# Performance work log

Measured on AMD Instinct MI355X. Metric: run time of the kernel, lower is better.

## Reference

```python
import jax, jax.numpy as jnp
import numpy as np
from jax import lax

# ---- static module constants (the torch module's registered buffers) ----
NRB = 8            # num_radial_basis
RAD = 2.5          # diameter / 2
GRID = 192         # voxel grid extent
N = 200000         # occupied voxels
DIM = 80           # 32x0e + 16x1o
ALPHA = 1.0 / np.sqrt(48.0)   # e3nn path normalization (fan_in = 32 + 16 into each output irrep)

_ax = np.arange(-2.0, 3.0, dtype=np.float32)                        # floor(2.5/1.0)=2 -> 5 taps/axis
LATTICE = np.stack(np.meshgrid(_ax, _ax, _ax, indexing='ij'), -1)   # [5,5,5,3]
PERM = np.arange(125).reshape(5, 5, 5).transpose(2, 1, 0).reshape(-1)  # einsum('xyz...->zyx...') as a flat permutation
OFFS = LATTICE.reshape(-1, 3).astype(np.int32)[PERM]                # voxel offsets, ordered to match permuted kernel


def _radial_emb():
    # soft_one_hot_linspace(..., basis='smooth_finite', cutoff=True)
    d = np.linalg.norm(LATTICE, axis=-1)
    centers = np.linspace(0.0, RAD, NRB + 2)[1:-1]
    step = centers[1] - centers[0]
    t = (d[..., None] - centers) / step
    inside = np.abs(t) < 1.0
    safe = np.where(inside, 1.0 - t * t, 1.0)
    return (1.14136 * np.exp(2.0) * np.where(inside, np.exp(-2.0 / safe), 0.0)).astype(np.float32)

EMB = _radial_emb().reshape(-1, NRB)  # [125, 8]


def _sph():
    # spherical harmonics l=0,1; normalize=True, normalization='component' (|Y_l|^2 = 2l+1)
    n = np.linalg.norm(LATTICE, axis=-1, keepdims=True)
    u = np.where(n > 0, LATTICE / np.maximum(n, 1e-9), 0.0)
    return np.concatenate([np.ones_like(n), np.sqrt(3.0) * u], -1).astype(np.float32)

SH = _sph().reshape(-1, 4)  # [125, 4]


def make_kernel(weight):
    # kernel(): (emb @ weight) / numel(lattice), then tp.right(sh, w) -> [tap, dim_in, dim_out]
    w = jnp.asarray(EMB) @ weight / 125.0        # [125, 2304]
    w1 = w[:, :1024].reshape(125, 32, 32)        # path 0e x 0e -> 0e
    w2 = w[:, 1024:1536].reshape(125, 32, 16)    # path 0e x 1o -> 1o
    w3 = w[:, 1536:1792].reshape(125, 16, 16)    # path 1o x 0e -> 1o
    w4 = w[:, 1792:].reshape(125, 16, 32)        # path 1o x 1o -> 0e (dot product)
    s0 = jnp.asarray(SH[:, 0])
    v = jnp.asarray(SH[:, 1:])
    eye3 = jnp.eye(3, dtype=w.dtype)
    K00 = ALPHA * w1 * s0[:, None, None]                                                  # [125,32,32]
    K01 = ALPHA * jnp.einsum('pik,pm->pikm', w2, v).reshape(125, 32, 48)                  # [125,32,48]
    K11 = ALPHA * jnp.einsum('pik,mn->pimkn', w3 * s0[:, None, None], eye3).reshape(125, 48, 48)
    K10 = (ALPHA / np.sqrt(3.0)) * jnp.einsum('pik,pm->pimk', w4, v).reshape(125, 48, 32)
    K = jnp.concatenate([jnp.concatenate([K00, K01], 2), jnp.concatenate([K10, K11], 2)], 1)
    return K[jnp.asarray(PERM)]  # xyz -> zyx tap order + flatten


def _forward(feats, weight, w_sc0, w_sc1, coords):
    kern = make_kernel(weight)  # [125, 80, 80]
    # residual e3nn Linear: per-irrep channel mixing with 1/sqrt(fan_in) normalization
    sc0 = feats[:, :32] @ (w_sc0 / np.sqrt(32.0))
    sc1 = jnp.einsum('nim,ik->nkm', feats[:, 32:].reshape(-1, 16, 3), w_sc1 / np.sqrt(16.0)).reshape(-1, 48)
    sc = jnp.concatenate([sc0, sc1], -1)
    # Minkowski sparse voxel conv: dense index volume -> per-tap gather / GEMM / accumulate
    n = coords.shape[0]
    idx_vol = jnp.full((GRID, GRID, GRID), -1, jnp.int32)
    idx_vol = idx_vol.at[coords[:, 0], coords[:, 1], coords[:, 2]].set(jnp.arange(n, dtype=jnp.int32))

    def tap(acc, oK):
        off, Ko = oK
        c = coords + off                                  # [N,3] neighbor coords for this tap
        ok = jnp.all((c >= 0) & (c < GRID), axis=1)
        cc = jnp.clip(c, 0, GRID - 1)
        nb = idx_vol[cc[:, 0], cc[:, 1], cc[:, 2]]        # [N] row index or -1
        f = jnp.where((ok & (nb >= 0))[:, None], feats[jnp.maximum(nb, 0)], 0.0)
        return acc + f @ Ko, None

    out, _ = lax.scan(tap, jnp.zeros(feats.shape, feats.dtype), (jnp.asarray(OFFS), kern))
    return sc + out


def setup_inputs() -> dict:
    key = jax.random.key(0)
    k1, k2, k3, k4 = jax.random.split(key, 4)
    rng = np.random.default_rng(0)
    lin = rng.choice(GRID ** 3, size=N, replace=False)  # unique occupied voxels
    coords = np.stack([lin // (GRID * GRID), (lin // GRID) % GRID, lin % GRID], 1).astype(np.int32)
    return {
        'feats': jax.random.normal(k1, (N, DIM), jnp.float32),
        'weight': jax.random.normal(k2, (NRB, 2304), jnp.float32),
        'w_sc0': jax.random.normal(k3, (32, 32), jnp.float32),
        'w_sc1': jax.random.normal(k4, (16, 16), jnp.float32),
        'coords': jnp.asarray(coords),
    }


def reference(feats, weight, w_sc0, w_sc1, coords):
    return _forward(feats, weight, w_sc0, w_sc1, coords)
```

## Files before the change

### kernel.cpp

```cpp
#include <hip/hip_runtime.h>

#define N_PTS 200000
#define GRIDL 192
#define CAP 8192
#define NREG 216
#define RCAP 1152
#define SCAP 96
#define HMAX 16
#define HCAP_TOT 524288

#define VOL_OFF   0ull
#define VOL_BYTES (192ull*192ull*192ull*4ull)
#define BINS_OFF  28311552ull
#define BCNT_OFF  36503552ull
#define GCUR_OFF  36519552ull
#define RCNT_OFF  36519680ull
#define PLIST_OFF 36547328ull
#define WBUF_OFF  38537984ull
#define VTAB_OFF  39689984ull
#define A0_OFF    39691984ull
#define A1_OFF    39696080ull
#define HDR_OFF   39697104ull
#define STAGE_OFF 41297104ull
#define WS_NEED   (STAGE_OFF + (unsigned long long)HCAP_TOT * 320ull)

struct TapTable { int p[80]; };
__host__ __device__ constexpr TapTable make_taps() {
    TapTable tt{}; int t = 0;
    for (int a = -2; a <= 2; a++)
        for (int b = -2; b <= 2; b++)
            for (int c = -2; c <= 2; c++) {
                int sq = a*a + b*b + c*c;
                if (sq >= 1 && sq <= 6) tt.p[t++] = (a+2)*25 + (b+2)*5 + (c+2);
            }
    return tt;
}
__device__ const TapTable TAPS = make_taps();

__global__ void prep_kernel(const float* __restrict__ wt, const float* __restrict__ wsc0,
                            const float* __restrict__ wsc1, float* __restrict__ wbuf,
                            float* __restrict__ vtab, float* __restrict__ A0,
                            float* __restrict__ A1) {
    int p = blockIdx.x;
    int dx = p / 25 - 2, dy = (p / 5) % 5 - 2, dz = p % 5 - 2;
    double d = sqrt((double)(dx*dx + dy*dy + dz*dz));
    const double step = 2.5 / 9.0;
    const double cst = 1.14136 * exp(2.0);
    float emb[8];
#pragma unroll
    for (int r = 0; r < 8; r++) {
        double t = (d - (double)(r + 1) * step) / step;
        double tt = t * t;
        emb[r] = (tt < 1.0) ? (float)(cst * exp(-2.0 / (1.0 - tt))) : 0.0f;
    }
    if (threadIdx.x == 0) {
        float inv = (d > 0.0) ? (float)(sqrt(3.0) / d) : 0.0f;
        vtab[p*4+0] = dx * inv; vtab[p*4+1] = dy * inv;
        vtab[p*4+2] = dz * inv; vtab[p*4+3] = 0.0f;
    }
    const float ALPHA = 0.14433756729740643f;
    for (int q = threadIdx.x; q < 2304; q += blockDim.x) {
        float acc = 0.0f;
#pragma unroll
        for (int r = 0; r < 8; r++) acc = fmaf(emb[r], wt[r*2304 + q], acc);
        acc *= (1.0f / 125.0f);
        float val = acc * ((q < 1792) ? ALPHA : (1.0f / 12.0f));
        wbuf[p*2304 + q] = val;
        if (p == 62) {
            if (q < 1024)                   A0[q]        = wsc0[q] * 0.17677669529663687f + val;
            else if (q >= 1536 && q < 1792) A1[q-1536]   = wsc1[q-1536] * 0.25f + val;
        }
    }
}

__global__ __launch_bounds__(256) void scatter_kernel(const int* __restrict__ coords,
        int* __restrict__ vol, int* __restrict__ rcnt_pad, int2* __restrict__ plist) {
    __shared__ int hist[216];
    __shared__ int rbase[216];
    for (int i = threadIdx.x; i < 216; i += 256) hist[i] = 0;
    __syncthreads();
    for (int n = blockIdx.x * 256 + threadIdx.x; n < N_PTS; n += 65536) {
        int x = coords[n*3], y = coords[n*3+1], z = coords[n*3+2];
        vol[(x * GRIDL + y) * GRIDL + z] = n;
        int r = (x >> 5) * 36 + (y >> 5) * 6 + (z >> 5);
        atomicAdd(&hist[r], 1);
    }
    __syncthreads();
    if (threadIdx.x < 216) {
        rbase[threadIdx.x] = atomicAdd(&rcnt_pad[threadIdx.x * 32], hist[threadIdx.x]);
        hist[threadIdx.x] = 0;
    }
    __syncthreads();
    for (int n = blockIdx.x * 256 + threadIdx.x; n < N_PTS; n += 65536) {
        int x = coords[n*3], y = coords[n*3+1], z = coords[n*3+2];
        int r = (x >> 5) * 36 + (y >> 5) * 6 + (z >> 5);
        int j = rbase[r] + atomicAdd(&hist[r], 1);
        if (j < RCAP) plist[r * RCAP + j] = make_int2(n, (x << 16) | (y << 8) | z);
    }
}

template<bool STG>
__global__ __launch_bounds__(256) void enum_kernel(const int* __restrict__ vol,
        const int* __restrict__ rcnt_pad, const int2* __restrict__ plist,
        int* __restrict__ bcnt_pad, int2* __restrict__ bins,
        int2* __restrict__ hdr, int* __restrict__ gcur) {
    int r = blockIdx.x;
    int cnt = min(rcnt_pad[r * 32], RCAP);
    __shared__ int hist[80];
    __shared__ int tbase[80];
    __shared__ int2 stage[80][SCAP];
    __shared__ int2 mh[STG ? 256 * HMAX : 1];
    __shared__ int blockTot;
    __shared__ int gbase_s;
    for (int i = threadIdx.x; i < 80; i += 256) hist[i] = 0;
    __syncthreads();

    for (int base = 0; base < cnt; base += 256) {
        int idx = base + threadIdx.x;
        bool act = idx < cnt;
        int n = -1, x = 0, y = 0, z = 0;
        if (act) {
            int2 e = plist[r * RCAP + idx];
            n = e.x; x = e.y >> 16; y = (e.y >> 8) & 255; z = e.y & 255;
        }
        int myc = 0;
        int t = 0;
#pragma unroll
        for (int a = -2; a <= 2; a++)
#pragma unroll
        for (int b = -2; b <= 2; b++)
#pragma unroll
        for (int c = -2; c <= 2; c++) {
            int sq = a*a + b*b + c*c;
            if (sq < 1 || sq > 6) continue;
            int cx = x + a, cy = y + b, cz = z + c;
            if (act && ((unsigned)cx < 192u) && ((unsigned)cy < 192u) && ((unsigned)cz < 192u)) {
                int nb = vol[(cx * GRIDL + cy) * GRIDL + cz];
                if (nb >= 0) {
                    if (STG) {
                        if (myc < HMAX) mh[threadIdx.x * HMAX + myc] = make_int2(t, nb);
                        myc++;
                    } else {
                        int j = atomicAdd(&hist[t], 1);
                        if (j < SCAP) stage[t][j] = make_int2(n, nb);
                    }
                }
            }
            t++;
        }
        if (STG) {
            myc = min(myc, HMAX);
            __syncthreads();
            if (threadIdx.x == 0) blockTot = 0;
            __syncthreads();
            int lbase = atomicAdd(&blockTot, myc);
            __syncthreads();
            if (threadIdx.x == 0) gbase_s = atomicAdd(gcur, blockTot);
            __syncthreads();
            int sbase = gbase_s + lbase;
            int avail = HCAP_TOT - sbase;
            int cn = min(myc, max(avail, 0));
            if (act) hdr[n] = make_int2(sbase, cn);
            for (int j = 0; j < cn; j++) {
                int2 e = mh[threadIdx.x * HMAX + j];
                int k = atomicAdd(&hist[e.x], 1);
                if (k < SCAP) stage[e.x][k] = make_int2(sbase + j, e.y);
            }
            __syncthreads();
        }
    }
    __syncthreads();
    if (threadIdx.x < 80) {
        int c = min(hist[threadIdx.x], SCAP);
        tbase[threadIdx.x] = atomicAdd(&bcnt_pad[TAPS.p[threadIdx.x] * 32], c);
    }
    __syncthreads();
    for (int t2 = 0; t2 < 80; t2++) {
        int c = min(hist[t2], SCAP);
        if (threadIdx.x < c) {
            int slot = tbase[t2] + threadIdx.x;
            if (slot < CAP) bins[TAPS.p[t2] * CAP + slot] = stage[t2][threadIdx.x];
        }
    }
}

__global__ __launch_bounds__(256) void sc_self_kernel(const float* __restrict__ feats,
        const float* __restrict__ A0, const float* __restrict__ A1,
        float* __restrict__ out) {
    __shared__ __align__(16) float sA0[1024];
    __shared__ __align__(16) float sA1[256];
    for (int i = threadIdx.x; i < 1024; i += 256) sA0[i] = A0[i];
    if (threadIdx.x < 256) sA1[threadIdx.x] = A1[threadIdx.x];
    __syncthreads();
    int n = blockIdx.x * 256 + threadIdx.x;
    if (n >= N_PTS) return;
    const float4* fr = (const float4*)(feats + (size_t)n * 80);
    float4* orow = (float4*)(out + (size_t)n * 80);
    float f0[32];
#pragma unroll
    for (int j = 0; j < 8; j++) {
        float4 t = fr[j];
        f0[4*j] = t.x; f0[4*j+1] = t.y; f0[4*j+2] = t.z; f0[4*j+3] = t.w;
    }
    float a0[32];
#pragma unroll
    for (int k = 0; k < 32; k++) a0[k] = 0.0f;
#pragma unroll
    for (int i = 0; i < 32; i++) {
        float fv = f0[i];
#pragma unroll
        for (int k4 = 0; k4 < 8; k4++) {
            float4 w = ((const float4*)sA0)[i*8 + k4];
            a0[4*k4]   = fmaf(fv, w.x, a0[4*k4]);
            a0[4*k4+1] = fmaf(fv, w.y, a0[4*k4+1]);
            a0[4*k4+2] = fmaf(fv, w.z, a0[4*k4+2]);
            a0[4*k4+3] = fmaf(fv, w.w, a0[4*k4+3]);
        }
    }
#pragma unroll
    for (int j = 0; j < 8; j++) orow[j] = make_float4(a0[4*j], a0[4*j+1], a0[4*j+2], a0[4*j+3]);
    float f1[48];
#pragma unroll
    for (int j = 0; j < 12; j++) {
        float4 t = fr[8 + j];
        f1[4*j] = t.x; f1[4*j+1] = t.y; f1[4*j+2] = t.z; f1[4*j+3] = t.w;
    }
    float a1[48];
#pragma unroll
    for (int k = 0; k < 48; k++) a1[k] = 0.0f;
#pragma unroll
    for (int i = 0; i < 16; i++) {
        float fm0 = f1[3*i], fm1 = f1[3*i+1], fm2 = f1[3*i+2];
#pragma unroll
        for (int k4 = 0; k4 < 4; k4++) {
            float4 w = ((const float4*)sA1)[i*4 + k4];
            const float* wp = (const float*)&w;
#pragma unroll
            for (int kk = 0; kk < 4; kk++) {
                int k = 4*k4 + kk;
                a1[3*k]   = fmaf(fm0, wp[kk], a1[3*k]);
                a1[3*k+1] = fmaf(fm1, wp[kk], a1[3*k+1]);
                a1[3*k+2] = fmaf(fm2, wp[kk], a1[3*k+2]);
            }
        }
    }
#pragma unroll
    for (int j = 0; j < 12; j++) orow[8+j] = make_float4(a1[4*j], a1[4*j+1], a1[4*j+2], a1[4*j+3]);
}

template<bool STG>
__global__ __launch_bounds__(128) void bin_kernel(const float* __restrict__ feats,
        const float* __restrict__ wbuf, const float* __restrict__ vtab,
        const int* __restrict__ bcnt_pad, const int2* __restrict__ bins,
        float* __restrict__ stg, float* __restrict__ out) {
    int p = blockIdx.x >> 4;
    int chunk = blockIdx.x & 15;
    int cnt = min(bcnt_pad[p * 32], CAP);
    int start = chunk * 512;
    if (start >= cnt) return;

    __shared__ __align__(16) float sW[2304];
    __shared__ float sv[4];
    __shared__ float ystage[2][64][81];
    __shared__ int   dst[2][64];

    for (int i = threadIdx.x; i < 2304; i += 128) sW[i] = wbuf[p*2304 + i];
    if (threadIdx.x < 4) sv[threadIdx.x] = vtab[p*4 + threadIdx.x];
    __syncthreads();

    int wv = threadIdx.x >> 6, lane = threadIdx.x & 63;
    const float4* sW1 = (const float4*)sW;
    const float4* sW2 = (const float4*)(sW + 1024);
    const float4* sW3 = (const float4*)(sW + 1536);
    const float4* sW4 = (const float4*)(sW + 1792);
    float v0 = sv[0], v1 = sv[1], v2 = sv[2];

    for (int it = 0; it < 4; it++) {
        int h = start + it * 128 + threadIdx.x;
        bool act = h < cnt;
        int d = -1, nb = 0;
        if (act) { int2 e = bins[p*CAP + h]; d = e.x; nb = e.y; }

        const float4* fr = (const float4*)(feats + (size_t)nb * 80);
        float f0[32], f1[48];
#pragma unroll
        for (int j = 0; j < 8; j++) {
            float4 t = fr[j];
            f0[4*j] = t.x; f0[4*j+1] = t.y; f0[4*j+2] = t.z; f0[4*j+3] = t.w;
        }
#pragma unroll
        for (int j = 0; j < 12; j++) {
            float4 t = fr[8 + j];
            f1[4*j] = t.x; f1[4*j+1] = t.y; f1[4*j+2] = t.z; f1[4*j+3] = t.w;
        }
        float g[16];
#pragma unroll
        for (int i = 0; i < 16; i++)
            g[i] = f1[3*i]*v0 + f1[3*i+1]*v1 + f1[3*i+2]*v2;

        float a0[32], cc[16];
#pragma unroll
        for (int k = 0; k < 32; k++) a0[k] = 0.0f;
#pragma unroll
        for (int k = 0; k < 16; k++) cc[k] = 0.0f;
#pragma unroll
        for (int i = 0; i < 32; i++) {
            float fv = f0[i];
#pragma unroll
            for (int k4 = 0; k4 < 8; k4++) {
                float4 w = sW1[i*8 + k4];
                a0[4*k4]   = fmaf(fv, w.x, a0[4*k4]);
                a0[4*k4+1] = fmaf(fv, w.y, a0[4*k4+1]);
                a0[4*k4+2] = fmaf(fv, w.z, a0[4*k4+2]);
                a0[4*k4+3] = fmaf(fv, w.w, a0[4*k4+3]);
            }
#pragma unroll
            for (int k4 = 0; k4 < 4; k4++) {
                float4 w = sW2[i*4 + k4];
                cc[4*k4]   = fmaf(fv, w.x, cc[4*k4]);
                cc[4*k4+1] = fmaf(fv, w.y, cc[4*k4+1]);
                cc[4*k4+2] = fmaf(fv, w.z, cc[4*k4+2]);
                cc[4*k4+3] = fmaf(fv, w.w, cc[4*k4+3]);
            }
        }
#pragma unroll
        for (int i = 0; i < 16; i++) {
            float gv = g[i];
#pragma unroll
            for (int k4 = 0; k4 < 8; k4++) {
                float4 w = sW4[i*8 + k4];
                a0[4*k4]   = fmaf(gv, w.x, a0[4*k4]);
                a0[4*k4+1] = fmaf(gv, w.y, a0[4*k4+1]);
                a0[4*k4+2] = fmaf(gv, w.z, a0[4*k4+2]);
                a0[4*k4+3] = fmaf(gv, w.w, a0[4*k4+3]);
            }
        }
#pragma unroll
        for (int k = 0; k < 32; k++) ystage[wv][lane][k] = a0[k];

        float a1[48];
#pragma unroll
        for (int k = 0; k < 16; k++) {
            a1[3*k] = v0 * cc[k]; a1[3*k+1] = v1 * cc[k]; a1[3*k+2] = v2 * cc[k];
        }
#pragma unroll
        for (int i = 0; i < 16; i++) {
            float fm0 = f1[3*i], fm1 = f1[3*i+1], fm2 = f1[3*i+2];
#pragma unroll
            for (int k4 = 0; k4 < 4; k4++) {
                float4 w = sW3[i*4 + k4];
                const float* wp = (const float*)&w;
#pragma unroll
                for (int kk = 0; kk < 4; kk++) {
                    int k = 4*k4 + kk;
                    a1[3*k]   = fmaf(fm0, wp[kk], a1[3*k]);
                    a1[3*k+1] = fmaf(fm1, wp[kk], a1[3*k+1]);
                    a1[3*k+2] = fmaf(fm2, wp[kk], a1[3*k+2]);
                }
            }
        }
#pragma unroll
        for (int k = 0; k < 48; k++) ystage[wv][lane][32 + k] = a1[k];
        dst[wv][lane] = act ? d : -1;
        __syncthreads();

        for (int h2 = 0; h2 < 64; h2++) {
            int dd = dst[wv][h2];
            if (dd < 0) continue;
            if (STG) {
                float* row = stg + (size_t)dd * 80;
                row[lane] = ystage[wv][h2][lane];
                if (lane < 16) row[64 + lane] = ystage[wv][h2][64 + lane];
            } else {
                float* orow = out + (size_t)dd * 80;
                unsafeAtomicAdd(orow + lane, ystage[wv][h2][lane]);
                if (lane < 16) unsafeAtomicAdd(orow + 64 + lane, ystage[wv][h2][64 + lane]);
            }
        }
        __syncthreads();
    }
}

__global__ __launch_bounds__(256) void gather_kernel(const float* __restrict__ feats,
        const float* __restrict__ A0, const float* __restrict__ A1,
        const int2* __restrict__ hdr, const float* __restrict__ stg,
        float* __restrict__ out) {
    __shared__ __align__(16) float sA0[1024];
    __shared__ __align__(16) float sA1[256];
    for (int i = threadIdx.x; i < 1024; i += 256) sA0[i] = A0[i];
    if (threadIdx.x < 256) sA1[threadIdx.x] = A1[threadIdx.x];
    __syncthreads();
    int n = blockIdx.x * 256 + threadIdx.x;
    if (n >= N_PTS) return;
    int2 h = hdr[n];
    const float4* fr = (const float4*)(feats + (size_t)n * 80);
    float a0[32], a1[48];
    {
        float f0[32];
#pragma unroll
        for (int j = 0; j < 8; j++) {
            float4 t = fr[j];
            f0[4*j] = t.x; f0[4*j+1] = t.y; f0[4*j+2] = t.z; f0[4*j+3] = t.w;
        }
#pragma unroll
        for (int k = 0; k < 32; k++) a0[k] = 0.0f;
#pragma unroll
        for (int i = 0; i < 32; i++) {
            float fv = f0[i];
#pragma unroll
            for (int k4 = 0; k4 < 8; k4++) {
                float4 w = ((const float4*)sA0)[i*8 + k4];
                a0[4*k4]   = fmaf(fv, w.x, a0[4*k4]);
                a0[4*k4+1] = fmaf(fv, w.y, a0[4*k4+1]);
                a0[4*k4+2] = fmaf(fv, w.z, a0[4*k4+2]);
                a0[4*k4+3] = fmaf(fv, w.w, a0[4*k4+3]);
            }
        }
        float f1[48];
#pragma unroll
        for (int j = 0; j < 12; j++) {
            float4 t = fr[8 + j];
            f1[4*j] = t.x; f1[4*j+1] = t.y; f1[4*j+2] = t.z; f1[4*j+3] = t.w;
        }
#pragma unroll
        for (int k = 0; k < 48; k++) a1[k] = 0.0f;
#pragma unroll
        for (int i = 0; i < 16; i++) {
            float fm0 = f1[3*i], fm1 = f1[3*i+1], fm2 = f1[3*i+2];
#pragma unroll
            for (int k4 = 0; k4 < 4; k4++) {
                float4 w = ((const float4*)sA1)[i*4 + k4];
                const float* wp = (const float*)&w;
#pragma unroll
                for (int kk = 0; kk < 4; kk++) {
                    int k = 4*k4 + kk;
                    a1[3*k]   = fmaf(fm0, wp[kk], a1[3*k]);
                    a1[3*k+1] = fmaf(fm1, wp[kk], a1[3*k+1]);
                    a1[3*k+2] = fmaf(fm2, wp[kk], a1[3*k+2]);
                }
            }
        }
    }
    for (int j = 0; j < h.y; j++) {
        const float4* rp = (const float4*)(stg + (size_t)(h.x + j) * 80);
#pragma unroll
        for (int q = 0; q < 8; q++) {
            float4 t = rp[q];
            a0[4*q] += t.x; a0[4*q+1] += t.y; a0[4*q+2] += t.z; a0[4*q+3] += t.w;
        }
#pragma unroll
        for (int q = 0; q < 12; q++) {
            float4 t = rp[8 + q];
            a1[4*q] += t.x; a1[4*q+1] += t.y; a1[4*q+2] += t.z; a1[4*q+3] += t.w;
        }
    }
    float4* orow = (float4*)(out + (size_t)n * 80);
#pragma unroll
    for (int j = 0; j < 8; j++)  orow[j]   = make_float4(a0[4*j], a0[4*j+1], a0[4*j+2], a0[4*j+3]);
#pragma unroll
    for (int j = 0; j < 12; j++) orow[8+j] = make_float4(a1[4*j], a1[4*j+1], a1[4*j+2], a1[4*j+3]);
}

extern "C" void kernel_launch(void* const* d_in, const int* in_sizes, int n_in,
                              void* d_out, int out_size, void* d_ws, size_t ws_size,
                              hipStream_t stream) {
    const float* feats = (const float*)d_in[0];
    const float* wt    = (const float*)d_in[1];
    const float* wsc0  = (const float*)d_in[2];
    const float* wsc1  = (const float*)d_in[3];
    const int*   coords= (const int*)d_in[4];
    float* out = (float*)d_out;
    char* ws = (char*)d_ws;

    int*   vol      = (int*)(ws + VOL_OFF);
    int2*  bins     = (int2*)(ws + BINS_OFF);
    int*   bcnt_pad = (int*)(ws + BCNT_OFF);
    int*   gcur     = (int*)(ws + GCUR_OFF);
    int*   rcnt_pad = (int*)(ws + RCNT_OFF);
    int2*  plist    = (int2*)(ws + PLIST_OFF);
    float* wbuf     = (float*)(ws + WBUF_OFF);
    float* vtab     = (float*)(ws + VTAB_OFF);
    float* A0       = (float*)(ws + A0_OFF);
    float* A1       = (float*)(ws + A1_OFF);
    int2*  hdr      = (int2*)(ws + HDR_OFF);
    float* stg      = (float*)(ws + STAGE_OFF);

    bool staging = (unsigned long long)ws_size >= WS_NEED;

    hipMemsetAsync(vol, 0xFF, VOL_BYTES, stream);
    hipMemsetAsync(bcnt_pad, 0, 16000 + 128 + 27648, stream);

    prep_kernel<<<125, 256, 0, stream>>>(wt, wsc0, wsc1, wbuf, vtab, A0, A1);
    scatter_kernel<<<256, 256, 0, stream>>>(coords, vol, rcnt_pad, plist);
    if (staging) {
        enum_kernel<true><<<NREG, 256, 0, stream>>>(vol, rcnt_pad, plist, bcnt_pad, bins, hdr, gcur);
        bin_kernel<true><<<125 * 16, 128, 0, stream>>>(feats, wbuf, vtab, bcnt_pad, bins, stg, out);
        gather_kernel<<<(N_PTS + 255) / 256, 256, 0, stream>>>(feats, A0, A1, hdr, stg, out);
    } else {
        enum_kernel<false><<<NREG, 256, 0, stream>>>(vol, rcnt_pad, plist, bcnt_pad, bins, hdr, gcur);
        sc_self_kernel<<<(N_PTS + 255) / 256, 256, 0, stream>>>(feats, A0, A1, out);
        bin_kernel<false><<<125 * 16, 128, 0, stream>>>(feats, wbuf, vtab, bcnt_pad, bins, stg, out);
    }
}
```

Baseline: 514.9 us.

## Split neighbor enumeration across region slices and write bin outputs directly

Neighbor enumeration now runs one 128-thread block per 128-point slice of each region instead of one 256-thread block per region. This spreads 216 large blocks over many more small ones, and the per-tap shared staging array gives way to a packed per-thread list with a two-pass count-then-place scheme. The bin kernel drops the shared-memory transpose and barrier-heavy per-row writeback: each thread writes its staged row with float4 stores, or with per-element atomics on the fallback path. Costs are more global atomics on the bin counters, less coalesced row stores, and packing that assumes neighbor indices fit in 18 bits.

Result: slower. 718.8 us (+39.6%).

```diff
diff --git a/kernel.cpp b/kernel.cpp
--- a/kernel.cpp
+++ b/kernel.cpp
@@ -5,7 +5,7 @@
 #define CAP 8192
 #define NREG 216
 #define RCAP 1152
-#define SCAP 96
+#define NSLICE 9
 #define HMAX 16
 #define HCAP_TOT 524288
 
@@ -87,7 +87,8 @@
     }
     __syncthreads();
     if (threadIdx.x < 216) {
-        rbase[threadIdx.x] = atomicAdd(&rcnt_pad[threadIdx.x * 32], hist[threadIdx.x]);
+        int c = hist[threadIdx.x];
+        rbase[threadIdx.x] = c ? atomicAdd(&rcnt_pad[threadIdx.x * 32], c) : 0;
         hist[threadIdx.x] = 0;
     }
     __syncthreads();
@@ -100,87 +101,77 @@
 }
 
 template<bool STG>
-__global__ __launch_bounds__(256) void enum_kernel(const int* __restrict__ vol,
+__global__ __launch_bounds__(128) void enum_kernel(const int* __restrict__ vol,
         const int* __restrict__ rcnt_pad, const int2* __restrict__ plist,
         int* __restrict__ bcnt_pad, int2* __restrict__ bins,
         int2* __restrict__ hdr, int* __restrict__ gcur) {
-    int r = blockIdx.x;
+    int r = blockIdx.x / NSLICE, s = blockIdx.x % NSLICE;
     int cnt = min(rcnt_pad[r * 32], RCAP);
+    int lo = s * 128, hi = min(cnt, lo + 128);
+    if (lo >= hi) return;
     __shared__ int hist[80];
     __shared__ int tbase[80];
-    __shared__ int2 stage[80][SCAP];
-    __shared__ int2 mh[STG ? 256 * HMAX : 1];
-    __shared__ int blockTot;
-    __shared__ int gbase_s;
-    for (int i = threadIdx.x; i < 80; i += 256) hist[i] = 0;
-    __syncthreads();
-
-    for (int base = 0; base < cnt; base += 256) {
-        int idx = base + threadIdx.x;
-        bool act = idx < cnt;
-        int n = -1, x = 0, y = 0, z = 0;
-        if (act) {
-            int2 e = plist[r * RCAP + idx];
-            n = e.x; x = e.y >> 16; y = (e.y >> 8) & 255; z = e.y & 255;
-        }
-        int myc = 0;
-        int t = 0;
-#pragma unroll
-        for (int a = -2; a <= 2; a++)
-#pragma unroll
-        for (int b = -2; b <= 2; b++)
-#pragma unroll
-        for (int c = -2; c <= 2; c++) {
-            int sq = a*a + b*b + c*c;
-            if (sq < 1 || sq > 6) continue;
-            int cx = x + a, cy = y + b, cz = z + c;
-            if (act && ((unsigned)cx < 192u) && ((unsigned)cy < 192u) && ((unsigned)cz < 192u)) {
-                int nb = vol[(cx * GRIDL + cy) * GRIDL + cz];
-                if (nb >= 0) {
-                    if (STG) {
-                        if (myc < HMAX) mh[threadIdx.x * HMAX + myc] = make_int2(t, nb);
-                        myc++;
-                    } else {
-                        int j = atomicAdd(&hist[t], 1);
-                        if (j < SCAP) stage[t][j] = make_int2(n, nb);
-                    }
-                }
-            }
-            t++;
-        }
-        if (STG) {
-            myc = min(myc, HMAX);
-            __syncthreads();
-            if (threadIdx.x == 0) blockTot = 0;
-            __syncthreads();
-            int lbase = atomicAdd(&blockTot, myc);
-            __syncthreads();
-            if (threadIdx.x == 0) gbase_s = atomicAdd(gcur, blockTot);
-            __syncthreads();
-            int sbase = gbase_s + lbase;
-            int avail = HCAP_TOT - sbase;
-            int cn = min(myc, max(avail, 0));
-            if (act) hdr[n] = make_int2(sbase, cn);
-            for (int j = 0; j < cn; j++) {
-                int2 e = mh[threadIdx.x * HMAX + j];
-                int k = atomicAdd(&hist[e.x], 1);
-                if (k < SCAP) stage[e.x][k] = make_int2(sbase + j, e.y);
-            }
-            __syncthreads();
-        }
-    }
-    __syncthreads();
-    if (threadIdx.x < 80) {
-        int c = min(hist[threadIdx.x], SCAP);
-        tbase[threadIdx.x] = atomicAdd(&bcnt_pad[TAPS.p[threadIdx.x] * 32], c);
-    }
-    __syncthreads();
-    for (int t2 = 0; t2 < 80; t2++) {
-        int c = min(hist[t2], SCAP);
-        if (threadIdx.x < c) {
-            int slot = tbase[t2] + threadIdx.x;
-            if (slot < CAP) bins[TAPS.p[t2] * CAP + slot] = stage[t2][threadIdx.x];
-        }
+    __shared__ int cursor[80];
+    __shared__ int mh[128 * HMAX];
+    __shared__ int blockTot, gbase_s;
+    if (threadIdx.x < 80) { hist[threadIdx.x] = 0; cursor[threadIdx.x] = 0; }
+    __syncthreads();
+
+    int idx = lo + threadIdx.x;
+    bool act = idx < hi;
+    int n = -1, x = 0, y = 0, z = 0;
+    if (act) {
+        int2 e = plist[r * RCAP + idx];
+        n = e.x; x = e.y >> 16; y = (e.y >> 8) & 255; z = e.y & 255;
+    }
+    int myc = 0;
+    int t = 0;
+#pragma unroll
+    for (int a = -2; a <= 2; a++)
+#pragma unroll
+    for (int b = -2; b <= 2; b++)
+#pragma unroll
+    for (int c = -2; c <= 2; c++) {
+        int sq = a*a + b*b + c*c;
+        if (sq < 1 || sq > 6) continue;
+        int cx = x + a, cy = y + b, cz = z + c;
+        if (act && ((unsigned)cx < 192u) && ((unsigned)cy < 192u) && ((unsigned)cz < 192u)) {
+            int nb = vol[(cx * GRIDL + cy) * GRIDL + cz];
+            if (nb >= 0 && myc < HMAX) {
+                mh[threadIdx.x * HMAX + myc] = (t << 18) | nb;
+                myc++;
+                atomicAdd(&hist[t], 1);
+            }
+        }
+        t++;
+    }
+    __syncthreads();
+
+    int sbase = 0, cn = myc;
+    if (STG) {
+        if (threadIdx.x == 0) blockTot = 0;
+        __syncthreads();
+        int lbase = atomicAdd(&blockTot, myc);
+        __syncthreads();
+        if (threadIdx.x == 0) gbase_s = atomicAdd(gcur, blockTot);
+        __syncthreads();
+        sbase = gbase_s + lbase;
+        int avail = HCAP_TOT - sbase;
+        cn = min(myc, max(avail, 0));
+        if (act) hdr[n] = make_int2(sbase, cn);
+    }
+    if (threadIdx.x < 80)
+        tbase[threadIdx.x] = hist[threadIdx.x]
+            ? atomicAdd(&bcnt_pad[TAPS.p[threadIdx.x] * 32], hist[threadIdx.x]) : 0;
+    __syncthreads();
+
+    for (int j = 0; j < cn; j++) {
+        int e = mh[threadIdx.x * HMAX + j];
+        int tt = e >> 18, nb = e & 0x3FFFF;
+        int k = atomicAdd(&cursor[tt], 1);
+        int pos = tbase[tt] + k;
+        if (pos < CAP)
+            bins[TAPS.p[tt] * CAP + pos] = make_int2(STG ? (sbase + j) : n, nb);
     }
 }
 
@@ -261,14 +252,10 @@
 
     __shared__ __align__(16) float sW[2304];
     __shared__ float sv[4];
-    __shared__ float ystage[2][64][81];
-    __shared__ int   dst[2][64];
-
     for (int i = threadIdx.x; i < 2304; i += 128) sW[i] = wbuf[p*2304 + i];
     if (threadIdx.x < 4) sv[threadIdx.x] = vtab[p*4 + threadIdx.x];
     __syncthreads();
 
-    int wv = threadIdx.x >> 6, lane = threadIdx.x & 63;
     const float4* sW1 = (const float4*)sW;
     const float4* sW2 = (const float4*)(sW + 1024);
     const float4* sW3 = (const float4*)(sW + 1536);
@@ -277,9 +264,9 @@
 
     for (int it = 0; it < 4; it++) {
         int h = start + it * 128 + threadIdx.x;
-        bool act = h < cnt;
-        int d = -1, nb = 0;
-        if (act) { int2 e = bins[p*CAP + h]; d = e.x; nb = e.y; }
+        if (h >= cnt) break;
+        int2 e = bins[p*CAP + h];
+        int d = e.x, nb = e.y;
 
         const float4* fr = (const float4*)(feats + (size_t)nb * 80);
         float f0[32], f1[48];
@@ -335,8 +322,16 @@
                 a0[4*k4+3] = fmaf(gv, w.w, a0[4*k4+3]);
             }
         }
-#pragma unroll
-        for (int k = 0; k < 32; k++) ystage[wv][lane][k] = a0[k];
+        if (STG) {
+            float4* row = (float4*)(stg + (size_t)d * 80);
+#pragma unroll
+            for (int j = 0; j < 8; j++)
+                row[j] = make_float4(a0[4*j], a0[4*j+1], a0[4*j+2], a0[4*j+3]);
+        } else {
+            float* orow = out + (size_t)d * 80;
+#pragma unroll
+            for (int k = 0; k < 32; k++) unsafeAtomicAdd(orow + k, a0[k]);
+        }
 
         float a1[48];
 #pragma unroll
@@ -359,25 +354,16 @@
                 }
             }
         }
-#pragma unroll
-        for (int k = 0; k < 48; k++) ystage[wv][lane][32 + k] = a1[k];
-        dst[wv][lane] = act ? d : -1;
-        __syncthreads();
-
-        for (int h2 = 0; h2 < 64; h2++) {
-            int dd = dst[wv][h2];
-            if (dd < 0) continue;
-            if (STG) {
-                float* row = stg + (size_t)dd * 80;
-                row[lane] = ystage[wv][h2][lane];
-                if (lane < 16) row[64 + lane] = ystage[wv][h2][64 + lane];
-            } else {
-                float* orow = out + (size_t)dd * 80;
-                unsafeAtomicAdd(orow + lane, ystage[wv][h2][lane]);
-                if (lane < 16) unsafeAtomicAdd(orow + 64 + lane, ystage[wv][h2][64 + lane]);
-            }
-        }
-        __syncthreads();
+        if (STG) {
+            float4* row = (float4*)(stg + (size_t)d * 80);
+#pragma unroll
+            for (int j = 0; j < 12; j++)
+                row[8+j] = make_float4(a1[4*j], a1[4*j+1], a1[4*j+2], a1[4*j+3]);
+        } else {
+            float* orow = out + (size_t)d * 80;
+#pragma unroll
+            for (int k = 0; k < 48; k++) unsafeAtomicAdd(orow + 32 + k, a1[k]);
+        }
     }
 }
 
@@ -493,11 +479,11 @@
     prep_kernel<<<125, 256, 0, stream>>>(wt, wsc0, wsc1, wbuf, vtab, A0, A1);
     scatter_kernel<<<256, 256, 0, stream>>>(coords, vol, rcnt_pad, plist);
     if (staging) {
-        enum_kernel<true><<<NREG, 256, 0, stream>>>(vol, rcnt_pad, plist, bcnt_pad, bins, hdr, gcur);
+        enum_kernel<true><<<NREG * NSLICE, 128, 0, stream>>>(vol, rcnt_pad, plist, bcnt_pad, bins, hdr, gcur);
         bin_kernel<true><<<125 * 16, 128, 0, stream>>>(feats, wbuf, vtab, bcnt_pad, bins, stg, out);
         gather_kernel<<<(N_PTS + 255) / 256, 256, 0, stream>>>(feats, A0, A1, hdr, stg, out);
     } else {
-        enum_kernel<false><<<NREG, 256, 0, stream>>>(vol, rcnt_pad, plist, bcnt_pad, bins, hdr, gcur);
+        enum_kernel<false><<<NREG * NSLICE, 128, 0, stream>>>(vol, rcnt_pad, plist, bcnt_pad, bins, hdr, gcur);
         sc_self_kernel<<<(N_PTS + 255) / 256, 256, 0, stream>>>(feats, A0, A1, out);
         bin_kernel<false><<<125 * 16, 128, 0, stream>>>(feats, wbuf, vtab, bcnt_pad, bins, stg, out);
     }
```
